# Kernel optimization log

Measured on AMD Instinct MI355X. Metric: run time of the kernel, lower is better.

## Reference

```python
import jax, jax.numpy as jnp
import numpy as np

B, S, D, H = 2, 2048, 1024, 16
DH = D // H  # key_dim = embed_dim // num_heads
NEG = 1e9    # Keras masked-softmax adder magnitude
EPS = 1e-6


def setup_inputs() -> dict:
    key = jax.random.key(0)
    ks = jax.random.split(key, 6)
    sc = 1.0 / np.sqrt(D)
    return {
        "x": jax.random.normal(ks[0], (B, S, D), jnp.float32),
        "Wq": jax.random.normal(ks[1], (D, H, DH), jnp.float32) * sc,
        "bq": jnp.zeros((H, DH), jnp.float32),
        "Wk": jax.random.normal(ks[2], (D, H, DH), jnp.float32) * sc,
        "bk": jnp.zeros((H, DH), jnp.float32),
        "Wv": jax.random.normal(ks[3], (D, H, DH), jnp.float32) * sc,
        "bv": jnp.zeros((H, DH), jnp.float32),
        "Wo": jax.random.normal(ks[4], (H, DH, D), jnp.float32) * (1.0 / np.sqrt(D)),
        "bo": jnp.zeros((D,), jnp.float32),
        "gamma": jnp.ones((D,), jnp.float32),
        "beta": jnp.zeros((D,), jnp.float32),
    }


def reference(x, Wq, bq, Wk, bk, Wv, bv, Wo, bo, gamma, beta):
    # Keras MultiHeadAttention(query=x, value=x), inference (dropouts are identity)
    q = jnp.einsum("bsd,dhk->bshk", x, Wq) + bq  # [B,S,H,DH]
    k = jnp.einsum("bsd,dhk->bshk", x, Wk) + bk
    v = jnp.einsum("bsd,dhk->bshk", x, Wv) + bv

    scores = jnp.einsum("bqhd,bkhd->bhqk", q, k) / jnp.sqrt(jnp.asarray(DH, x.dtype))
    # Source: mask = 1 - band_part(ones, -1, 0) -> ones strictly ABOVE diagonal.
    # Keras attends where mask==1 and adds (1-mask)*(-1e9) elsewhere. Faithful:
    i = jnp.arange(S)[:, None]
    j = jnp.arange(S)[None, :]
    allowed = (j > i).astype(scores.dtype)  # [S,S], strict upper triangle
    scores = scores + (allowed - 1.0) * NEG  # subtract 1e9 where not allowed
    probs = jax.nn.softmax(scores, axis=-1)

    ctx = jnp.einsum("bhqk,bkhd->bqhd", probs, v)  # [B,S,H,DH]
    attn_out = jnp.einsum("bqhd,hdo->bqo", ctx, Wo) + bo  # [B,S,D]

    # residual + LayerNorm(eps=1e-6)
    y = x + attn_out
    mu = jnp.mean(y, axis=-1, keepdims=True)
    var = jnp.mean(jnp.square(y - mu), axis=-1, keepdims=True)
    return (y - mu) * jax.lax.rsqrt(var + EPS) * gamma + beta
```

## Files before the change

### kernel.cpp

```cpp
#include <hip/hip_runtime.h>
#include <hip/hip_bf16.h>

typedef __hip_bfloat16 bf16;
typedef __attribute__((ext_vector_type(8))) short bf16x8;
typedef __attribute__((ext_vector_type(4))) float f32x4;

constexpr int Bc  = 2;
constexpr int Sc  = 2048;
constexpr int Dc  = 1024;
constexpr int Hc  = 16;
constexpr int DHc = 64;
constexpr int BS  = Bc * Sc;
constexpr int NT  = Sc / 64;

__device__ __forceinline__ float bs2f(unsigned short u) {
    union { unsigned int i; float f; } v; v.i = ((unsigned int)u) << 16; return v.f;
}
__device__ __forceinline__ short f2bs(float x) {
    bf16 h = __float2bfloat16(x);
    return *reinterpret_cast<short*>(&h);
}

typedef const __attribute__((address_space(1))) unsigned int* as1_u32p;
typedef __attribute__((address_space(3))) unsigned int* as3_u32p;
__device__ __forceinline__ void gl_lds16(const void* g, void* l) {
    __builtin_amdgcn_global_load_lds((as1_u32p)g, (as3_u32p)l, 16, 0, 0);
}

__global__ __launch_bounds__(256) void prep(
    const float* __restrict__ x, short* __restrict__ xb,
    const float* __restrict__ w0, const float* __restrict__ w1,
    const float* __restrict__ w2, const float* __restrict__ w3,
    short* __restrict__ WT)
{
    __shared__ float T[64][65];
    const int i = blockIdx.x;
    const int t = threadIdx.x;

    if (i < 4096) {
        const int off = i * 1024 + t * 4;
        const float4 v = *(const float4*)(x + off);
        ushort4 o;
        o.x = (unsigned short)f2bs(v.x);
        o.y = (unsigned short)f2bs(v.y);
        o.z = (unsigned short)f2bs(v.z);
        o.w = (unsigned short)f2bs(v.w);
        *(ushort4*)(xb + off) = o;
        return;
    }

    const int idx = i - 4096;
    const int z  = idx >> 8;
    const int k0 = (idx & 15) * 64;
    const int n0 = ((idx >> 4) & 15) * 64;
    const float* in = (z == 0) ? w0 : (z == 1) ? w1 : (z == 2) ? w2 : w3;
    short* out = WT + (size_t)z * 1024 * 1024;
    #pragma unroll
    for (int it = 0; it < 4; ++it) {
        const int s = it * 256 + t;
        const int r = s >> 4, c = (s & 15) * 4;
        *(float4*)&T[r][c] = *(const float4*)(in + (size_t)(k0 + r) * 1024 + n0 + c);
    }
    __syncthreads();
    #pragma unroll
    for (int it = 0; it < 4; ++it) {
        const int s = it * 256 + t;
        const int rr = s >> 4, cc = (s & 15) * 4;
        ushort4 o;
        o.x = (unsigned short)f2bs(T[cc + 0][rr]);
        o.y = (unsigned short)f2bs(T[cc + 1][rr]);
        o.z = (unsigned short)f2bs(T[cc + 2][rr]);
        o.w = (unsigned short)f2bs(T[cc + 3][rr]);
        *(ushort4*)(out + (size_t)(n0 + rr) * 1024 + k0 + cc) = o;
    }
}

__global__ __launch_bounds__(256, 3) void gemm_bt(
    const short* __restrict__ A, const short* __restrict__ BTbase,
    const float* __restrict__ b0, const float* __restrict__ b1,
    const float* __restrict__ b2, short* __restrict__ Cbase,
    const float sc0)
{
    __shared__ __align__(16) short As[128 * 64];
    __shared__ __align__(16) short Bs[128 * 64];

    const int z = blockIdx.z;
    const short* BT = BTbase + (size_t)z * 1024 * 1024;
    const float* bias = (z == 0) ? b0 : (z == 1) ? b1 : b2;
    const float sc = (z == 0) ? sc0 : 1.0f;
    short* C = Cbase + (size_t)z * BS * Dc;

    const int t = threadIdx.x;
    const int lane = t & 63, w = t >> 6;
    const int quad = lane >> 4, l16 = lane & 15;
    const int wm = (w & 1) * 64, wn = (w >> 1) * 64;
    const int row0 = blockIdx.y * 128;
    const int col0 = blockIdx.x * 128;
    const int sw = l16 & 7;

    f32x4 acc[4][4] = {};

    for (int kt = 0; kt < 1024; kt += 64) {
        __syncthreads();
        #pragma unroll
        for (int i = 0; i < 4; ++i) {
            const int f = i * 256 + t;
            const int r = f >> 3;
            const int g = (f & 7) ^ (r & 7);
            short* lb = &As[(i * 256 + w * 64) * 8];
            gl_lds16(A + (size_t)(row0 + r) * 1024 + kt + g * 8, lb);
            short* lb2 = &Bs[(i * 256 + w * 64) * 8];
            gl_lds16(BT + (size_t)(col0 + r) * 1024 + kt + g * 8, lb2);
        }
        __syncthreads();
        #pragma unroll
        for (int ks = 0; ks < 2; ++ks) {
            bf16x8 av[4], bv[4];
            #pragma unroll
            for (int mt = 0; mt < 4; ++mt) {
                const int r = wm + mt * 16 + l16;
                av[mt] = *(const bf16x8*)&As[r * 64 + ((ks * 4 + quad) ^ sw) * 8];
            }
            #pragma unroll
            for (int nt = 0; nt < 4; ++nt) {
                const int r = wn + nt * 16 + l16;
                bv[nt] = *(const bf16x8*)&Bs[r * 64 + ((ks * 4 + quad) ^ sw) * 8];
            }
            #pragma unroll
            for (int mt = 0; mt < 4; ++mt)
                #pragma unroll
                for (int nt = 0; nt < 4; ++nt)
                    acc[mt][nt] = __builtin_amdgcn_mfma_f32_16x16x32_bf16(
                        av[mt], bv[nt], acc[mt][nt], 0, 0, 0);
        }
    }

    float bvv[4];
    #pragma unroll
    for (int nt = 0; nt < 4; ++nt) bvv[nt] = bias[col0 + wn + nt * 16 + l16];
    #pragma unroll
    for (int mt = 0; mt < 4; ++mt)
        #pragma unroll
        for (int reg = 0; reg < 4; ++reg) {
            const size_t row = row0 + wm + mt * 16 + quad * 4 + reg;
            #pragma unroll
            for (int nt = 0; nt < 4; ++nt) {
                const int col = col0 + wn + nt * 16 + l16;
                C[row * 1024 + col] = f2bs((acc[mt][nt][reg] + bvv[nt]) * sc);
            }
        }
}


template<bool DIAG>
__device__ __forceinline__ void qtile_step(
    const bf16x8 (&qf)[2],
    const short (&Ks)[64][72], const short (&VsT)[64][72],
    short (&Psw)[16][72],
    const int k0, const int row_base,
    const int quad, const int l16,
    const bf16x8 ones,
    f32x4 &lacc, f32x4 (&O)[4])
{
    bf16x8 kf[2][4];
    #pragma unroll
    for (int ks = 0; ks < 2; ++ks)
        #pragma unroll
        for (int nt = 0; nt < 4; ++nt)
            kf[ks][nt] = *(const bf16x8*)&Ks[nt * 16 + l16][ks * 32 + quad * 8];

    f32x4 S[4] = {};
    __builtin_amdgcn_s_setprio(1);
    #pragma unroll
    for (int ks = 0; ks < 2; ++ks)
        #pragma unroll
        for (int nt = 0; nt < 4; ++nt)
            S[nt] = __builtin_amdgcn_mfma_f32_16x16x32_bf16(qf[ks], kf[ks][nt], S[nt], 0, 0, 0);
    __builtin_amdgcn_s_setprio(0);

    #pragma unroll
    for (int nt = 0; nt < 4; ++nt) {
        #pragma unroll
        for (int reg = 0; reg < 4; ++reg) {
            float s = fminf(S[nt][reg], 115.4f);
            if (DIAG) {
                const int col = k0 + nt * 16 + l16;
                const int row = row_base + quad * 4 + reg;
                s = (col > row) ? s : -126.0f;
            }
            S[nt][reg] = exp2f(s);
        }
    }

    #pragma unroll
    for (int reg = 0; reg < 4; ++reg) {
        const __hip_bfloat162 lo = __float22bfloat162_rn(make_float2(S[0][reg], S[1][reg]));
        const __hip_bfloat162 hi = __float22bfloat162_rn(make_float2(S[2][reg], S[3][reg]));
        uint2 u;
        u.x = *reinterpret_cast<const unsigned int*>(&lo);
        u.y = *reinterpret_cast<const unsigned int*>(&hi);
        *(uint2*)&Psw[quad * 4 + reg][l16 * 4] = u;
    }

    __builtin_amdgcn_s_setprio(1);
    #pragma unroll
    for (int ks = 0; ks < 2; ++ks) {
        const bf16x8 pf = *(const bf16x8*)&Psw[l16][ks * 32 + quad * 8];
        lacc = __builtin_amdgcn_mfma_f32_16x16x32_bf16(pf, ones, lacc, 0, 0, 0);
        #pragma unroll
        for (int nt = 0; nt < 4; ++nt) {
            const bf16x8 vf = *(const bf16x8*)&VsT[nt * 16 + l16][ks * 32 + quad * 8];
            O[nt] = __builtin_amdgcn_mfma_f32_16x16x32_bf16(pf, vf, O[nt], 0, 0, 0);
        }
    }
    __builtin_amdgcn_s_setprio(0);
}

__global__ __launch_bounds__(256, 3) void attn_mfma(
    const short* __restrict__ Qg, const short* __restrict__ Kg,
    const short* __restrict__ Vg, short* __restrict__ CTX)
{
    __shared__ __align__(16) short Ks [2][64][72];
    __shared__ __align__(16) short VsT[2][64][72];
    __shared__ __align__(16) short Ps[4][16][72];
    __shared__ float red[4][64];

    const int tid  = threadIdx.x;

    if (blockIdx.y == 16) {
        const int h = blockIdx.x, b = blockIdx.z;
        const int dh = tid & 63, ck = tid >> 6;
        float s = 0.f;
        const short* vp = Vg + ((size_t)b * Sc + ck * 512) * Dc + h * DHc + dh;
        for (int j = 0; j < 512; ++j) s += bs2f(vp[(size_t)j * Dc]);
        red[ck][dh] = s;
        __syncthreads();
        if (ck == 0) {
            const float tot = (red[0][dh] + red[1][dh] + red[2][dh] + red[3][dh]) * (1.f / Sc);
            CTX[((size_t)b * Sc + Sc - 1) * Dc + h * DHc + dh] = f2bs(tot);
        }
        return;
    }

    const int lane = tid & 63, w = tid >> 6;
    const int quad = lane >> 4, l16 = lane & 15;

    const int xcd   = blockIdx.x & 7;
    const int local = (blockIdx.x >> 3) + 2 * blockIdx.y + 32 * blockIdx.z;
    const int bh    = xcd * 4 + (local >> 4);
    const int p     = local & 15;
    const int h     = bh & 15;
    const int b     = bh >> 4;
    const size_t rb = (size_t)b * Sc;
    const int cb = h * DHc;

    const int skey = tid & 63, sseg = (tid >> 6) * 8;
    const int pkey = ((skey & 15) << 2) | (skey >> 4);

    bf16x8 ones;
    #pragma unroll
    for (int e = 0; e < 8; ++e) ones[e] = (short)0x3F80;

    const size_t tstride = (size_t)64 * Dc;

    #pragma unroll 1
    for (int ph = 0; ph < 2; ++ph) {
        const int myq = ph ? (NT - 1 - p) : p;
        const int t0  = myq;
        const int q0  = myq * 64;

        bf16x8 qf[2];
        {
            const short* qp = Qg + (rb + q0 + w * 16 + l16) * (size_t)Dc + cb + quad * 8;
            qf[0] = *(const bf16x8*)(qp);
            qf[1] = *(const bf16x8*)(qp + 32);
        }
        f32x4 lacc = {};
        f32x4 O[4] = {};

        const short* kp = Kg + (rb + (size_t)t0 * 64 + skey) * Dc + cb + sseg;
        const short* vp = Vg + (rb + (size_t)t0 * 64 + skey) * Dc + cb + sseg;

        if (ph) __syncthreads();

        {
            const int buf = t0 & 1;
            const bf16x8 k0v = *(const bf16x8*)(kp);
            const bf16x8 k1v = *(const bf16x8*)(kp + 32);
            const bf16x8 v0v = *(const bf16x8*)(vp);
            const bf16x8 v1v = *(const bf16x8*)(vp + 32);
            *(bf16x8*)&Ks[buf][skey][sseg]      = k0v;
            *(bf16x8*)&Ks[buf][skey][sseg + 32] = k1v;
            #pragma unroll
            for (int e = 0; e < 8; ++e) {
                VsT[buf][sseg + e][pkey]      = v0v[e];
                VsT[buf][sseg + 32 + e][pkey] = v1v[e];
            }
        }
        __syncthreads();

        for (int t = t0; t < NT; ++t) {
            const int cur = t & 1;
            const bool havenext = (t + 1 < NT);
            bf16x8 pk0, pk1, pv0, pv1;
            if (havenext) {
                pk0 = *(const bf16x8*)(kp + tstride);
                pk1 = *(const bf16x8*)(kp + tstride + 32);
                pv0 = *(const bf16x8*)(vp + tstride);
                pv1 = *(const bf16x8*)(vp + tstride + 32);
            }

            if (t == t0)
                qtile_step<true >(qf, Ks[cur], VsT[cur], Ps[w],
                                  t * 64, q0 + w * 16, quad, l16, ones, lacc, O);
            else
                qtile_step<false>(qf, Ks[cur], VsT[cur], Ps[w],
                                  t * 64, q0 + w * 16, quad, l16, ones, lacc, O);

            if (havenext) {
                const int nb = cur ^ 1;
                *(bf16x8*)&Ks[nb][skey][sseg]      = pk0;
                *(bf16x8*)&Ks[nb][skey][sseg + 32] = pk1;
                #pragma unroll
                for (int e = 0; e < 8; ++e) {
                    VsT[nb][sseg + e][pkey]      = pv0[e];
                    VsT[nb][sseg + 32 + e][pkey] = pv1[e];
                }
                __syncthreads();
            }
            kp += tstride;
            vp += tstride;
        }

        float inv[4];
        #pragma unroll
        for (int reg = 0; reg < 4; ++reg) inv[reg] = 1.0f / lacc[reg];
        #pragma unroll
        for (int nt = 0; nt < 4; ++nt)
            #pragma unroll
            for (int reg = 0; reg < 4; ++reg) {
                const int lr = q0 + w * 16 + quad * 4 + reg;
                if (lr != Sc - 1)
                    CTX[(rb + lr) * Dc + cb + nt * 16 + l16] = f2bs(O[nt][reg] * inv[reg]);
            }
    }
}

__global__ __launch_bounds__(256, 4) void resid_ln(
    const float* __restrict__ X, const short* __restrict__ AO,
    const float* __restrict__ gamma, const float* __restrict__ beta,
    float* __restrict__ out)
{
    const int r = blockIdx.x;
    const int t = threadIdx.x;
    const size_t base = (size_t)r * Dc + t * 4;

    const float4 x4 = *(const float4*)(X + base);
    const ushort4 a4 = *(const ushort4*)(AO + base);
    float y[4];
    y[0] = x4.x + bs2f(a4.x);
    y[1] = x4.y + bs2f(a4.y);
    y[2] = x4.z + bs2f(a4.z);
    y[3] = x4.w + bs2f(a4.w);

    float s  = y[0] + y[1] + y[2] + y[3];
    float s2 = y[0]*y[0] + y[1]*y[1] + y[2]*y[2] + y[3]*y[3];
    #pragma unroll
    for (int off = 1; off < 64; off <<= 1) {
        s  += __shfl_xor(s,  off, 64);
        s2 += __shfl_xor(s2, off, 64);
    }
    __shared__ float red[8];
    const int w = t >> 6;
    if ((t & 63) == 0) { red[w] = s; red[4 + w] = s2; }
    __syncthreads();
    s  = red[0] + red[1] + red[2] + red[3];
    s2 = red[4] + red[5] + red[6] + red[7];

    const float mu   = s * (1.0f / Dc);
    const float rstd = rsqrtf(s2 * (1.0f / Dc) - mu * mu + 1e-6f);

    const float4 g4 = *(const float4*)(gamma + t * 4);
    const float4 b4 = *(const float4*)(beta  + t * 4);
    float4 o;
    o.x = (y[0] - mu) * rstd * g4.x + b4.x;
    o.y = (y[1] - mu) * rstd * g4.y + b4.y;
    o.z = (y[2] - mu) * rstd * g4.z + b4.z;
    o.w = (y[3] - mu) * rstd * g4.w + b4.w;
    *(float4*)(out + base) = o;
}

extern "C" void kernel_launch(void* const* d_in, const int* in_sizes, int n_in,
                              void* d_out, int out_size, void* d_ws, size_t ws_size,
                              hipStream_t stream)
{
    (void)in_sizes; (void)n_in; (void)out_size; (void)ws_size;
    const float* x     = (const float*)d_in[0];
    const float* Wq    = (const float*)d_in[1];
    const float* bq    = (const float*)d_in[2];
    const float* Wk    = (const float*)d_in[3];
    const float* bk    = (const float*)d_in[4];
    const float* Wv    = (const float*)d_in[5];
    const float* bv    = (const float*)d_in[6];
    const float* Wo    = (const float*)d_in[7];
    const float* bo    = (const float*)d_in[8];
    const float* gamma = (const float*)d_in[9];
    const float* beta  = (const float*)d_in[10];
    float* out = (float*)d_out;

    const size_t matN = (size_t)BS * Dc;
    const size_t wN   = (size_t)Dc * Dc;
    short* xb = (short*)d_ws;
    short* WT = xb + matN;
    short* Qb = WT + 4 * wN;
    short* Kb = Qb + matN;
    short* Vb = Kb + matN;
    short* Cx = Vb + matN;
    short* AO = Qb;

    prep<<<5120, 256, 0, stream>>>(x, xb, Wq, Wk, Wv, Wo, WT);

    dim3 gq(Dc / 128, BS / 128, 3);
    gemm_bt<<<gq, 256, 0, stream>>>(xb, WT, bq, bk, bv, Qb, 0.18033688f);

    dim3 ga(16, 17, 2);
    attn_mfma<<<ga, 256, 0, stream>>>(Qb, Kb, Vb, Cx);

    dim3 go(Dc / 128, BS / 128, 1);
    gemm_bt<<<go, 256, 0, stream>>>(Cx, WT + 3 * wN, bo, bo, bo, AO, 1.0f);

    resid_ln<<<BS, 256, 0, stream>>>(x, AO, gamma, beta, out);
}
```

Baseline: 203.3 us.

## Load K fragments directly to registers and use narrower output-projection GEMM tiles

The attention kernel stops staging K tiles through shared memory. Each wave now loads its K MFMA fragments straight from global memory into registers and prefetches the next tile while the current one is computed. This removes the LDS stores and reads for K but makes every wave fetch K redundantly from global or cache memory. The output projection GEMM switches to a new 128x64 tile kernel, which doubles the block count to improve occupancy and load balance at the cost of less reuse per block.

```diff
diff --git a/kernel.cpp b/kernel.cpp
--- a/kernel.cpp
+++ b/kernel.cpp
@@ -151,76 +151,84 @@
         }
 }
 
-
-template<bool DIAG>
-__device__ __forceinline__ void qtile_step(
-    const bf16x8 (&qf)[2],
-    const short (&Ks)[64][72], const short (&VsT)[64][72],
-    short (&Psw)[16][72],
-    const int k0, const int row_base,
-    const int quad, const int l16,
-    const bf16x8 ones,
-    f32x4 &lacc, f32x4 (&O)[4])
-{
-    bf16x8 kf[2][4];
-    #pragma unroll
-    for (int ks = 0; ks < 2; ++ks)
-        #pragma unroll
-        for (int nt = 0; nt < 4; ++nt)
-            kf[ks][nt] = *(const bf16x8*)&Ks[nt * 16 + l16][ks * 32 + quad * 8];
-
-    f32x4 S[4] = {};
-    __builtin_amdgcn_s_setprio(1);
-    #pragma unroll
-    for (int ks = 0; ks < 2; ++ks)
-        #pragma unroll
-        for (int nt = 0; nt < 4; ++nt)
-            S[nt] = __builtin_amdgcn_mfma_f32_16x16x32_bf16(qf[ks], kf[ks][nt], S[nt], 0, 0, 0);
-    __builtin_amdgcn_s_setprio(0);
-
-    #pragma unroll
-    for (int nt = 0; nt < 4; ++nt) {
+__global__ __launch_bounds__(256, 3) void gemm_bt_n64(
+    const short* __restrict__ A, const short* __restrict__ BT,
+    const float* __restrict__ bias, short* __restrict__ C)
+{
+    __shared__ __align__(16) short As[128 * 64];
+    __shared__ __align__(16) short Bs[64 * 64];
+
+    const int t = threadIdx.x;
+    const int lane = t & 63, w = t >> 6;
+    const int quad = lane >> 4, l16 = lane & 15;
+    const int wm = (w & 1) * 64, wn = (w >> 1) * 32;
+    const int row0 = blockIdx.y * 128;
+    const int col0 = blockIdx.x * 64;
+    const int sw = l16 & 7;
+
+    f32x4 acc[4][2] = {};
+
+    for (int kt = 0; kt < 1024; kt += 64) {
+        __syncthreads();
+        #pragma unroll
+        for (int i = 0; i < 4; ++i) {
+            const int f = i * 256 + t;
+            const int r = f >> 3;
+            const int g = (f & 7) ^ (r & 7);
+            gl_lds16(A + (size_t)(row0 + r) * 1024 + kt + g * 8,
+                     &As[(i * 256 + w * 64) * 8]);
+        }
+        #pragma unroll
+        for (int i = 0; i < 2; ++i) {
+            const int f = i * 256 + t;
+            const int r = f >> 3;
+            const int g = (f & 7) ^ (r & 7);
+            gl_lds16(BT + (size_t)(col0 + r) * 1024 + kt + g * 8,
+                     &Bs[(i * 256 + w * 64) * 8]);
+        }
+        __syncthreads();
+        #pragma unroll
+        for (int ks = 0; ks < 2; ++ks) {
+            bf16x8 av[4], bv[2];
+            #pragma unroll
+            for (int mt = 0; mt < 4; ++mt) {
+                const int r = wm + mt * 16 + l16;
+                av[mt] = *(const bf16x8*)&As[r * 64 + ((ks * 4 + quad) ^ sw) * 8];
+            }
+            #pragma unroll
+            for (int nt = 0; nt < 2; ++nt) {
+                const int r = wn + nt * 16 + l16;
+                bv[nt] = *(const bf16x8*)&Bs[r * 64 + ((ks * 4 + quad) ^ sw) * 8];
+            }
+            #pragma unroll
+            for (int mt = 0; mt < 4; ++mt)
+                #pragma unroll
+                for (int nt = 0; nt < 2; ++nt)
+                    acc[mt][nt] = __builtin_amdgcn_mfma_f32_16x16x32_bf16(
+                        av[mt], bv[nt], acc[mt][nt], 0, 0, 0);
+        }
+    }
+
+    float bvv[2];
+    #pragma unroll
+    for (int nt = 0; nt < 2; ++nt) bvv[nt] = bias[col0 + wn + nt * 16 + l16];
+    #pragma unroll
+    for (int mt = 0; mt < 4; ++mt)
         #pragma unroll
         for (int reg = 0; reg < 4; ++reg) {
-            float s = fminf(S[nt][reg], 115.4f);
-            if (DIAG) {
-                const int col = k0 + nt * 16 + l16;
-                const int row = row_base + quad * 4 + reg;
-                s = (col > row) ? s : -126.0f;
-            }
-            S[nt][reg] = exp2f(s);
-        }
-    }
-
-    #pragma unroll
-    for (int reg = 0; reg < 4; ++reg) {
-        const __hip_bfloat162 lo = __float22bfloat162_rn(make_float2(S[0][reg], S[1][reg]));
-        const __hip_bfloat162 hi = __float22bfloat162_rn(make_float2(S[2][reg], S[3][reg]));
-        uint2 u;
-        u.x = *reinterpret_cast<const unsigned int*>(&lo);
-        u.y = *reinterpret_cast<const unsigned int*>(&hi);
-        *(uint2*)&Psw[quad * 4 + reg][l16 * 4] = u;
-    }
-
-    __builtin_amdgcn_s_setprio(1);
-    #pragma unroll
-    for (int ks = 0; ks < 2; ++ks) {
-        const bf16x8 pf = *(const bf16x8*)&Psw[l16][ks * 32 + quad * 8];
-        lacc = __builtin_amdgcn_mfma_f32_16x16x32_bf16(pf, ones, lacc, 0, 0, 0);
-        #pragma unroll
-        for (int nt = 0; nt < 4; ++nt) {
-            const bf16x8 vf = *(const bf16x8*)&VsT[nt * 16 + l16][ks * 32 + quad * 8];
-            O[nt] = __builtin_amdgcn_mfma_f32_16x16x32_bf16(pf, vf, O[nt], 0, 0, 0);
-        }
-    }
-    __builtin_amdgcn_s_setprio(0);
+            const size_t row = row0 + wm + mt * 16 + quad * 4 + reg;
+            #pragma unroll
+            for (int nt = 0; nt < 2; ++nt) {
+                const int col = col0 + wn + nt * 16 + l16;
+                C[row * 1024 + col] = f2bs(acc[mt][reg == reg ? nt : nt][reg] + bvv[nt]);
+            }
+        }
 }
 
 __global__ __launch_bounds__(256, 3) void attn_mfma(
     const short* __restrict__ Qg, const short* __restrict__ Kg,
     const short* __restrict__ Vg, short* __restrict__ CTX)
 {
-    __shared__ __align__(16) short Ks [2][64][72];
     __shared__ __align__(16) short VsT[2][64][72];
     __shared__ __align__(16) short Ps[4][16][72];
     __shared__ float red[4][64];
@@ -278,19 +286,22 @@
         f32x4 lacc = {};
         f32x4 O[4] = {};
 
-        const short* kp = Kg + (rb + (size_t)t0 * 64 + skey) * Dc + cb + sseg;
+        const short* kfp = Kg + (rb + (size_t)t0 * 64 + l16) * Dc + cb + quad * 8;
         const short* vp = Vg + (rb + (size_t)t0 * 64 + skey) * Dc + cb + sseg;
+
+        bf16x8 kf[2][4];
+        #pragma unroll
+        for (int ks = 0; ks < 2; ++ks)
+            #pragma unroll
+            for (int nt = 0; nt < 4; ++nt)
+                kf[ks][nt] = *(const bf16x8*)(kfp + (size_t)nt * 16 * Dc + ks * 32);
 
         if (ph) __syncthreads();
 
         {
             const int buf = t0 & 1;
-            const bf16x8 k0v = *(const bf16x8*)(kp);
-            const bf16x8 k1v = *(const bf16x8*)(kp + 32);
             const bf16x8 v0v = *(const bf16x8*)(vp);
             const bf16x8 v1v = *(const bf16x8*)(vp + 32);
-            *(bf16x8*)&Ks[buf][skey][sseg]      = k0v;
-            *(bf16x8*)&Ks[buf][skey][sseg + 32] = k1v;
             #pragma unroll
             for (int e = 0; e < 8; ++e) {
                 VsT[buf][sseg + e][pkey]      = v0v[e];
@@ -302,25 +313,70 @@
         for (int t = t0; t < NT; ++t) {
             const int cur = t & 1;
             const bool havenext = (t + 1 < NT);
-            bf16x8 pk0, pk1, pv0, pv1;
+            bf16x8 pv0, pv1;
             if (havenext) {
-                pk0 = *(const bf16x8*)(kp + tstride);
-                pk1 = *(const bf16x8*)(kp + tstride + 32);
                 pv0 = *(const bf16x8*)(vp + tstride);
                 pv1 = *(const bf16x8*)(vp + tstride + 32);
             }
 
-            if (t == t0)
-                qtile_step<true >(qf, Ks[cur], VsT[cur], Ps[w],
-                                  t * 64, q0 + w * 16, quad, l16, ones, lacc, O);
-            else
-                qtile_step<false>(qf, Ks[cur], VsT[cur], Ps[w],
-                                  t * 64, q0 + w * 16, quad, l16, ones, lacc, O);
+            f32x4 S[4] = {};
+            __builtin_amdgcn_s_setprio(1);
+            #pragma unroll
+            for (int ks = 0; ks < 2; ++ks)
+                #pragma unroll
+                for (int nt = 0; nt < 4; ++nt)
+                    S[nt] = __builtin_amdgcn_mfma_f32_16x16x32_bf16(
+                        qf[ks], kf[ks][nt], S[nt], 0, 0, 0);
+            __builtin_amdgcn_s_setprio(0);
+
+            if (havenext) {
+                const short* kp_ = kfp + tstride;
+                #pragma unroll
+                for (int ks = 0; ks < 2; ++ks)
+                    #pragma unroll
+                    for (int nt = 0; nt < 4; ++nt)
+                        kf[ks][nt] = *(const bf16x8*)(kp_ + (size_t)nt * 16 * Dc + ks * 32);
+            }
+
+            #pragma unroll
+            for (int nt = 0; nt < 4; ++nt) {
+                #pragma unroll
+                for (int reg = 0; reg < 4; ++reg) {
+                    float s = fminf(S[nt][reg], 115.4f);
+                    if (t == t0) {
+                        const int col = t * 64 + nt * 16 + l16;
+                        const int row = q0 + w * 16 + quad * 4 + reg;
+                        s = (col > row) ? s : -126.0f;
+                    }
+                    S[nt][reg] = exp2f(s);
+                }
+            }
+
+            #pragma unroll
+            for (int reg = 0; reg < 4; ++reg) {
+                const __hip_bfloat162 lo = __float22bfloat162_rn(make_float2(S[0][reg], S[1][reg]));
+                const __hip_bfloat162 hi = __float22bfloat162_rn(make_float2(S[2][reg], S[3][reg]));
+                uint2 u;
+                u.x = *reinterpret_cast<const unsigned int*>(&lo);
+                u.y = *reinterpret_cast<const unsigned int*>(&hi);
+                *(uint2*)&Ps[w][quad * 4 + reg][l16 * 4] = u;
+            }
+
+            __builtin_amdgcn_s_setprio(1);
+            #pragma unroll
+            for (int ks = 0; ks < 2; ++ks) {
+                const bf16x8 pf = *(const bf16x8*)&Ps[w][l16][ks * 32 + quad * 8];
+                lacc = __builtin_amdgcn_mfma_f32_16x16x32_bf16(pf, ones, lacc, 0, 0, 0);
+                #pragma unroll
+                for (int nt = 0; nt < 4; ++nt) {
+                    const bf16x8 vf = *(const bf16x8*)&VsT[cur][nt * 16 + l16][ks * 32 + quad * 8];
+                    O[nt] = __builtin_amdgcn_mfma_f32_16x16x32_bf16(pf, vf, O[nt], 0, 0, 0);
+                }
+            }
+            __builtin_amdgcn_s_setprio(0);
 
             if (havenext) {
                 const int nb = cur ^ 1;
-                *(bf16x8*)&Ks[nb][skey][sseg]      = pk0;
-                *(bf16x8*)&Ks[nb][skey][sseg + 32] = pk1;
                 #pragma unroll
                 for (int e = 0; e < 8; ++e) {
                     VsT[nb][sseg + e][pkey]      = pv0[e];
@@ -328,8 +384,8 @@
                 }
                 __syncthreads();
             }
-            kp += tstride;
-            vp += tstride;
+            kfp += tstride;
+            vp  += tstride;
         }
 
         float inv[4];
@@ -426,8 +482,8 @@
     dim3 ga(16, 17, 2);
     attn_mfma<<<ga, 256, 0, stream>>>(Qb, Kb, Vb, Cx);
 
-    dim3 go(Dc / 128, BS / 128, 1);
-    gemm_bt<<<go, 256, 0, stream>>>(Cx, WT + 3 * wN, bo, bo, bo, AO, 1.0f);
+    dim3 go(Dc / 64, BS / 128, 1);
+    gemm_bt_n64<<<go, 256, 0, stream>>>(Cx, WT + 3 * wN, bo, AO);
 
     resid_ln<<<BS, 256, 0, stream>>>(x, AO, gamma, beta, out);
 }
```

Measured after the change: 226.7 us. 11.5% more time.
